# Performance work log

Measured on AMD Instinct MI355X. Metric: run time of the kernel, lower is better.

## Reference

```python
import jax, jax.numpy as jnp
import numpy as np

B = 2048       # batch
D_IN = 512     # input_size
D_MODEL = 1024 # hidden_size / d_model
ED = 2048      # d_inner = 2*d_model
N = 16         # d_state
K = 4          # d_conv
DT = 64        # dt_rank = ceil(d_model/16)
FLAT_H = ED * N
RMS_EPS = 1e-5


def setup_inputs() -> dict:
    key = jax.random.key(0)
    ks = jax.random.split(key, 12)
    rn = lambda k, shape, s: jax.random.normal(k, shape, jnp.float32) * s
    return {
        "x_t": rn(ks[0], (B, D_IN), 1.0),
        "flat_state": rn(ks[1], (B, FLAT_H + ED * (K - 1)), 0.1),
        "W_in_cell": rn(ks[2], (D_MODEL, D_IN), D_IN ** -0.5),
        "norm_w": jnp.ones((D_MODEL,), jnp.float32),
        "W_in": rn(ks[3], (2 * ED, D_MODEL), D_MODEL ** -0.5),
        "conv_w": rn(ks[4], (ED, K), K ** -0.5),  # depthwise conv weight (ED,1,K) squeezed
        "conv_b": rn(ks[5], (ED,), 0.02),
        "W_xproj": rn(ks[6], (DT + 2 * N, ED), ED ** -0.5),
        "W_dt": rn(ks[7], (ED, DT), DT ** -0.5),
        "b_dt": rn(ks[8], (ED,), 0.02),
        "A_log": jnp.log(jnp.broadcast_to(jnp.arange(1, N + 1, dtype=jnp.float32), (ED, N))),
        "D_param": jnp.ones((ED,), jnp.float32),
        "W_out": rn(ks[9], (D_MODEL, ED), ED ** -0.5),
    }


def _rmsnorm(x, w):
    return x * jax.lax.rsqrt(jnp.mean(x * x, axis=-1, keepdims=True) + RMS_EPS) * w


def reference(x_t, flat_state, W_in_cell, norm_w, W_in, conv_w, conv_b,
              W_xproj, W_dt, b_dt, A_log, D_param, W_out):
    # MambaCell.in_proj (bias=False)
    x = x_t @ W_in_cell.T                                  # (B, D_MODEL)
    # unpack flat recurrent state
    h = flat_state[:, :FLAT_H].reshape(B, ED, N)           # SSM state
    inputs = flat_state[:, FLAT_H:].reshape(B, ED, K - 1)  # conv cache

    residual = x
    xn = _rmsnorm(x, norm_w)

    # MambaBlock.step
    xz = xn @ W_in.T                                       # (B, 2*ED)
    x1, z = xz[:, :ED], xz[:, ED:]

    # depthwise causal conv, last output position only
    window = jnp.concatenate([inputs, x1[:, :, None]], axis=2)   # (B, ED, K)
    xc = jnp.einsum("bek,ek->be", window, conv_w) + conv_b
    xs = jax.nn.silu(xc)                                   # (B, ED)

    # selective SSM single step
    dbc = xs @ W_xproj.T                                   # (B, DT+2N)
    delta = jax.nn.softplus(dbc[:, :DT] @ W_dt.T + b_dt)   # (B, ED)
    Bm = dbc[:, DT:DT + N]                                 # (B, N)
    Cm = dbc[:, DT + N:]                                   # (B, N)
    A = -jnp.exp(A_log)                                    # (ED, N)
    dA = jnp.exp(delta[:, :, None] * A[None])              # (B, ED, N)
    dBx = delta[:, :, None] * Bm[:, None, :] * xs[:, :, None]
    h_new = dA * h + dBx                                   # (B, ED, N)
    y = jnp.einsum("ben,bn->be", h_new, Cm) + D_param * xs

    out = (y * jax.nn.silu(z)) @ W_out.T                   # (B, D_MODEL)
    y_t = out + residual                                   # residual connection in ResidualBlock.step

    inputs_new = jnp.concatenate([inputs[:, :, 1:], x1[:, :, None]], axis=2)
    flat_new = jax.lax.stop_gradient(
        jnp.concatenate([h_new.reshape(B, -1), inputs_new.reshape(B, -1)], axis=1))
    return y_t, flat_new
```

## Files before the change

kernel.cpp:

```cpp
#include <hip/hip_runtime.h>
#include <math.h>

#define B 2048
#define D_IN 512
#define D_MODEL 1024
#define ED 2048
#define NSTATE 16
#define KCONV 4
#define DTDIM 64
#define FLAT_H (ED * NSTATE)
#define ROW_STATE (FLAT_H + ED * (KCONV - 1))

typedef __attribute__((ext_vector_type(8))) short short8;
typedef __attribute__((ext_vector_type(4))) short short4v;
typedef __attribute__((ext_vector_type(4))) float f32x4;

__device__ __forceinline__ float sigmoidf_(float x) { return 1.f / (1.f + expf(-x)); }

__device__ __forceinline__ unsigned short f2bf(float f) {
  unsigned u = __float_as_uint(f);
  u += 0x7FFFu + ((u >> 16) & 1u);
  return (unsigned short)(u >> 16);
}
__device__ __forceinline__ float bf2f(unsigned short h) {
  return __uint_as_float((unsigned)h << 16);
}

template <int MODE>
__global__ __launch_bounds__(256) void gemm_nt_mfma(
    const float* __restrict__ A, const float* __restrict__ W,
    float* __restrict__ C, int M, int N, int K, int lda, int ldw, int ldc,
    const float* __restrict__ extra) {
  __shared__ short Ahi[4][128][8];
  __shared__ short Alo[4][128][8];
  __shared__ short Whi[4][128][8];
  __shared__ short Wlo[4][128][8];

  const int tid = threadIdx.x;
  const int lane = tid & 63;
  const int wave = tid >> 6;
  const int wr = wave >> 1;
  const int wc = wave & 1;
  const int m0 = blockIdx.y * 128;
  const int n0 = blockIdx.x * 128;
  const int kg = lane >> 4;
  const int lr = lane & 15;

  f32x4 acc[4][4] = {};

  for (int k0 = 0; k0 < K; k0 += 32) {
#pragma unroll
    for (int it = 0; it < 4; ++it) {
      const int flat = tid + it * 256;
      const int row = flat >> 3;
      const int kq = flat & 7;
      const int tkg = kq >> 1;
      const int j0 = (kq & 1) * 4;
      const float4 av = *(const float4*)(A + (size_t)(m0 + row) * lda + (k0 + kq * 4));
      const float4 wv = *(const float4*)(W + (size_t)(n0 + row) * ldw + (k0 + kq * 4));
      const float af[4] = {av.x, av.y, av.z, av.w};
      const float wf[4] = {wv.x, wv.y, wv.z, wv.w};
      short4v ah, al, wh, wl;
#pragma unroll
      for (int e = 0; e < 4; ++e) {
        const unsigned short h = f2bf(af[e]);
        ah[e] = (short)h;
        al[e] = (short)f2bf(af[e] - bf2f(h));
        const unsigned short hw = f2bf(wf[e]);
        wh[e] = (short)hw;
        wl[e] = (short)f2bf(wf[e] - bf2f(hw));
      }
      *(short4v*)&Ahi[tkg][row][j0] = ah;
      *(short4v*)&Alo[tkg][row][j0] = al;
      *(short4v*)&Whi[tkg][row][j0] = wh;
      *(short4v*)&Wlo[tkg][row][j0] = wl;
    }
    __syncthreads();

    short8 a_h[4], a_l[4], b_h[4], b_l[4];
#pragma unroll
    for (int i = 0; i < 4; ++i) {
      a_h[i] = *(const short8*)&Ahi[kg][wr * 64 + i * 16 + lr][0];
      a_l[i] = *(const short8*)&Alo[kg][wr * 64 + i * 16 + lr][0];
      b_h[i] = *(const short8*)&Whi[kg][wc * 64 + i * 16 + lr][0];
      b_l[i] = *(const short8*)&Wlo[kg][wc * 64 + i * 16 + lr][0];
    }
#pragma unroll
    for (int i = 0; i < 4; ++i)
#pragma unroll
      for (int j = 0; j < 4; ++j) {
        acc[i][j] = __builtin_amdgcn_mfma_f32_16x16x32_bf16(a_h[i], b_h[j], acc[i][j], 0, 0, 0);
        acc[i][j] = __builtin_amdgcn_mfma_f32_16x16x32_bf16(a_l[i], b_h[j], acc[i][j], 0, 0, 0);
        acc[i][j] = __builtin_amdgcn_mfma_f32_16x16x32_bf16(a_h[i], b_l[j], acc[i][j], 0, 0, 0);
      }
    __syncthreads();
  }

#pragma unroll
  for (int i = 0; i < 4; ++i) {
    const int gm = m0 + wr * 64 + i * 16 + kg * 4;
#pragma unroll
    for (int j = 0; j < 4; ++j) {
      const int gn = n0 + wc * 64 + j * 16 + lr;
#pragma unroll
      for (int r = 0; r < 4; ++r) {
        float v = acc[i][j][r];
        if (MODE == 1) {
          v += extra[gn];
          v = (v > 20.f) ? v : log1pf(expf(v));
        } else if (MODE == 2) {
          v += extra[(size_t)(gm + r) * ldc + gn];
        }
        C[(size_t)(gm + r) * ldc + gn] = v;
      }
    }
  }
}

__global__ __launch_bounds__(256) void gemm_nt_splitk(
    const float* __restrict__ A, const float* __restrict__ W,
    float* __restrict__ C, int M, int N, int K, int lda, int ldw, int ldc) {
  __shared__ float As[16][68];
  __shared__ float Ws[16][68];
  const int tid = threadIdx.x;
  const int tx = tid & 15;
  const int ty = tid >> 4;
  const int m0 = blockIdx.y * 64;
  const int n0 = blockIdx.x * 64;
  const int kchunk = K / gridDim.z;
  const int kbeg = blockIdx.z * kchunk;

  float acc[4][4] = {};
  const int lr = tid >> 4;
  const int lc = tid & 15;

  for (int k0 = kbeg; k0 < kbeg + kchunk; k0 += 16) {
#pragma unroll
    for (int i = 0; i < 4; i++) {
      const int r = lr + i * 16;
      const int gk = k0 + lc;
      As[lc][r] = A[(size_t)(m0 + r) * lda + gk];
      const int gn = n0 + r;
      Ws[lc][r] = (gn < N) ? W[(size_t)gn * ldw + gk] : 0.f;
    }
    __syncthreads();
#pragma unroll
    for (int k = 0; k < 16; k++) {
      float a[4], w[4];
#pragma unroll
      for (int i = 0; i < 4; i++) a[i] = As[k][ty * 4 + i];
#pragma unroll
      for (int j = 0; j < 4; j++) w[j] = Ws[k][tx * 4 + j];
#pragma unroll
      for (int i = 0; i < 4; i++)
#pragma unroll
        for (int j = 0; j < 4; j++) acc[i][j] += a[i] * w[j];
    }
    __syncthreads();
  }

#pragma unroll
  for (int i = 0; i < 4; i++) {
    const int gm = m0 + ty * 4 + i;
#pragma unroll
    for (int j = 0; j < 4; j++) {
      const int gn = n0 + tx * 4 + j;
      if (gn >= N) continue;
      atomicAdd(&C[(size_t)gm * ldc + gn], acc[i][j]);
    }
  }
}

__global__ __launch_bounds__(256) void rmsnorm_kernel(
    const float* __restrict__ x, const float* __restrict__ w,
    float* __restrict__ xn) {
  const int b = blockIdx.x;
  const int i4 = threadIdx.x * 4;
  const float4 v = *(const float4*)(x + (size_t)b * D_MODEL + i4);
  float ss = v.x * v.x + v.y * v.y + v.z * v.z + v.w * v.w;
#pragma unroll
  for (int off = 32; off > 0; off >>= 1) ss += __shfl_down(ss, off, 64);
  __shared__ float red[4];
  if ((threadIdx.x & 63) == 0) red[threadIdx.x >> 6] = ss;
  __syncthreads();
  const float tot = red[0] + red[1] + red[2] + red[3];
  const float scale = rsqrtf(tot * (1.f / (float)D_MODEL) + 1e-5f);
  const float4 wv = *(const float4*)(w + i4);
  float4 o;
  o.x = v.x * scale * wv.x;
  o.y = v.y * scale * wv.y;
  o.z = v.z * scale * wv.z;
  o.w = v.w * scale * wv.w;
  *(float4*)(xn + (size_t)b * D_MODEL + i4) = o;
}

__global__ __launch_bounds__(256) void prep_aneg(
    const float* __restrict__ A_log, float* __restrict__ Aneg) {
  const int i4 = (blockIdx.x * 256 + threadIdx.x) * 4;
  const float4 v = *(const float4*)(A_log + i4);
  float4 o;
  o.x = -expf(v.x);
  o.y = -expf(v.y);
  o.z = -expf(v.z);
  o.w = -expf(v.w);
  *(float4*)(Aneg + i4) = o;
}

__global__ __launch_bounds__(256) void conv_silu_kernel(
    const float* __restrict__ flat_state, const float* __restrict__ xz,
    const float* __restrict__ conv_w, const float* __restrict__ conv_b,
    float* __restrict__ xs, float* __restrict__ outFlat) {
  const int b = blockIdx.x;
  __shared__ float sin_[ED * 3];
  __shared__ float sx1[ED];
  const float* inRow = flat_state + (size_t)b * ROW_STATE + FLAT_H;
  const float* x1Row = xz + (size_t)b * (2 * ED);
#pragma unroll
  for (int i = 0; i < 6; ++i) {
    const int idx = (threadIdx.x + i * 256) * 4;
    *(float4*)&sin_[idx] = *(const float4*)&inRow[idx];
  }
#pragma unroll
  for (int i = 0; i < 2; ++i) {
    const int idx = (threadIdx.x + i * 256) * 4;
    *(float4*)&sx1[idx] = *(const float4*)&x1Row[idx];
  }
  __syncthreads();
  float* xsRow = xs + (size_t)b * ED;
#pragma unroll
  for (int k = 0; k < 8; ++k) {
    const int e = threadIdx.x + k * 256;
    const float4 cw = *(const float4*)(conv_w + e * 4);
    const float xc = sin_[e * 3] * cw.x + sin_[e * 3 + 1] * cw.y +
                     sin_[e * 3 + 2] * cw.z + sx1[e] * cw.w + conv_b[e];
    xsRow[e] = xc * sigmoidf_(xc);
  }
  float* on = outFlat + (size_t)b * ROW_STATE + FLAT_H;
#pragma unroll
  for (int k = 0; k < 24; ++k) {
    const int i = threadIdx.x + k * 256;
    const int q = i / 3;
    const int r = i - q * 3;
    on[i] = (r == 2) ? sx1[q] : sin_[i + 1];
  }
}

__global__ __launch_bounds__(256) void state_kernel(
    const float* __restrict__ flat_state, const float* __restrict__ xz,
    const float* __restrict__ xs, const float* __restrict__ dbc,
    const float* __restrict__ delta, const float* __restrict__ Aneg,
    const float* __restrict__ D_param, float* __restrict__ outFlat,
    float* __restrict__ yz) {
  const int id = blockIdx.x * 256 + threadIdx.x;
  const int f = id << 2;
  const int b = f >> 15;
  const int off = f & 32767;
  const int e = off >> 4;
  const int n0 = off & 15;

  const float d = delta[(size_t)b * ED + e];
  const float xsv = xs[(size_t)b * ED + e];
  const float dx = d * xsv;
  const float4 h4 = *(const float4*)(flat_state + (size_t)b * ROW_STATE + off);
  const float4 a4 = *(const float4*)(Aneg + off);
  const float* dbcb = dbc + (size_t)b * 96;
  const float4 B4 = *(const float4*)(dbcb + DTDIM + n0);
  const float4 C4 = *(const float4*)(dbcb + DTDIM + NSTATE + n0);

  float4 hn;
  hn.x = expf(d * a4.x) * h4.x + dx * B4.x;
  hn.y = expf(d * a4.y) * h4.y + dx * B4.y;
  hn.z = expf(d * a4.z) * h4.z + dx * B4.z;
  hn.w = expf(d * a4.w) * h4.w + dx * B4.w;
  *(float4*)(outFlat + (size_t)b * ROW_STATE + off) = hn;

  float y = hn.x * C4.x + hn.y * C4.y + hn.z * C4.z + hn.w * C4.w;
  y += __shfl_xor(y, 1, 64);
  y += __shfl_xor(y, 2, 64);
  if (n0 == 0) {
    y += D_param[e] * xsv;
    const float z = xz[(size_t)b * (2 * ED) + ED + e];
    yz[(size_t)b * ED + e] = y * (z * sigmoidf_(z));
  }
}

extern "C" void kernel_launch(void* const* d_in, const int* in_sizes, int n_in,
                              void* d_out, int out_size, void* d_ws, size_t ws_size,
                              hipStream_t stream) {
  const float* x_t       = (const float*)d_in[0];
  const float* flat_state= (const float*)d_in[1];
  const float* W_in_cell = (const float*)d_in[2];
  const float* norm_w    = (const float*)d_in[3];
  const float* W_in      = (const float*)d_in[4];
  const float* conv_w    = (const float*)d_in[5];
  const float* conv_b    = (const float*)d_in[6];
  const float* W_xproj   = (const float*)d_in[7];
  const float* W_dt      = (const float*)d_in[8];
  const float* b_dt      = (const float*)d_in[9];
  const float* A_log     = (const float*)d_in[10];
  const float* D_param   = (const float*)d_in[11];
  const float* W_out     = (const float*)d_in[12];

  float* y_t_out = (float*)d_out;
  float* outFlat = (float*)d_out + (size_t)B * D_MODEL;

  float* ws = (float*)d_ws;
  float* x     = ws;
  float* xn    = x + (size_t)B * D_MODEL;
  float* xz    = xn + (size_t)B * D_MODEL;
  float* xs    = xz + (size_t)B * 2 * ED;
  float* dbc   = xs + (size_t)B * ED;
  float* delta = dbc + (size_t)B * 96;
  float* yz    = delta + (size_t)B * ED;
  float* Aneg  = xn;

  dim3 blk(256);

  (void)hipMemsetAsync(dbc, 0, (size_t)B * 96 * sizeof(float), stream);

  gemm_nt_mfma<0><<<dim3(D_MODEL / 128, B / 128), blk, 0, stream>>>(
      x_t, W_in_cell, x, B, D_MODEL, D_IN, D_IN, D_IN, D_MODEL, nullptr);
  rmsnorm_kernel<<<dim3(B), blk, 0, stream>>>(x, norm_w, xn);
  gemm_nt_mfma<0><<<dim3(2 * ED / 128, B / 128), blk, 0, stream>>>(
      xn, W_in, xz, B, 2 * ED, D_MODEL, D_MODEL, D_MODEL, 2 * ED, nullptr);
  prep_aneg<<<dim3(ED * NSTATE / 1024), blk, 0, stream>>>(A_log, Aneg);
  conv_silu_kernel<<<dim3(B), blk, 0, stream>>>(
      flat_state, xz, conv_w, conv_b, xs, outFlat);
  gemm_nt_splitk<<<dim3(2, B / 64, 8), blk, 0, stream>>>(
      xs, W_xproj, dbc, B, 96, ED, ED, ED, 96);
  gemm_nt_mfma<1><<<dim3(ED / 128, B / 128), blk, 0, stream>>>(
      dbc, W_dt, delta, B, ED, DTDIM, 96, DTDIM, ED, b_dt);
  state_kernel<<<dim3((size_t)B * FLAT_H / 1024), blk, 0, stream>>>(
      flat_state, xz, xs, dbc, delta, Aneg, D_param, outFlat, yz);
  gemm_nt_mfma<2><<<dim3(D_MODEL / 128, B / 128), blk, 0, stream>>>(
      yz, W_out, y_t_out, B, D_MODEL, ED, ED, ED, D_MODEL, x);
}
```

Baseline: 909.7 us.

## Pre-split operands to bf16 hi/lo and load GEMM tiles via global_load_lds

Adds split kernels that convert the inputs, weights and activations into separate bf16 high and low arrays once. A new GEMM then streams these tiles directly into swizzled LDS with global_load_lds, instead of converting fp32 to split bf16 inside every GEMM tile load. This is meant to remove the repeated per-tile conversion ALU work and halve the global bytes read per operand. In exchange it adds extra launches and extra global traffic for the split passes, including re-splitting the weights on every call.

```diff
diff --git a/kernel.cpp b/kernel.cpp
--- a/kernel.cpp
+++ b/kernel.cpp
@@ -14,6 +14,7 @@
 typedef __attribute__((ext_vector_type(8))) short short8;
 typedef __attribute__((ext_vector_type(4))) short short4v;
 typedef __attribute__((ext_vector_type(4))) float f32x4;
+typedef unsigned short ushort_t;
 
 __device__ __forceinline__ float sigmoidf_(float x) { return 1.f / (1.f + expf(-x)); }
 
@@ -24,6 +25,116 @@
 }
 __device__ __forceinline__ float bf2f(unsigned short h) {
   return __uint_as_float((unsigned)h << 16);
+}
+struct hl_t { short h, l; };
+__device__ __forceinline__ hl_t split2(float f) {
+  hl_t r;
+  const unsigned short hu = f2bf(f);
+  r.h = (short)hu;
+  r.l = (short)f2bf(f - bf2f(hu));
+  return r;
+}
+
+__device__ __forceinline__ void gload_lds16(const void* g, void* l) {
+  __builtin_amdgcn_global_load_lds(
+      (const __attribute__((address_space(1))) void*)g,
+      (__attribute__((address_space(3))) void*)l, 16, 0, 0);
+}
+
+template <int MODE>
+__global__ __launch_bounds__(256) void gemm_bs(
+    const ushort_t* __restrict__ Ahi, const ushort_t* __restrict__ Alo,
+    const ushort_t* __restrict__ Whi, const ushort_t* __restrict__ Wlo,
+    float* __restrict__ C, int M, int N, int K, int ldc,
+    const float* __restrict__ extra) {
+  __shared__ ushort_t lds[2][128][64];
+
+  const int tid = threadIdx.x;
+  const int lane = tid & 63;
+  const int w = tid >> 6;
+  const int wr = w >> 1;
+  const int wc = w & 1;
+  const int m0 = blockIdx.y * 128;
+  const int n0 = blockIdx.x * 128;
+  const int kg = lane >> 4;
+  const int lr = lane & 15;
+
+  const int srow = lane >> 3;
+  const int sslot = lane & 7;
+  const int c = sslot ^ srow;
+  const int mat = c >> 2;
+  const int kq8 = (c & 3) * 8;
+
+  const int side = w >> 1;
+  const ushort_t* hiP = side ? Whi : Ahi;
+  const ushort_t* loP = side ? Wlo : Alo;
+  const ushort_t* matP = mat ? loP : hiP;
+  const int base0 = side ? n0 : m0;
+
+  f32x4 acc[4][4] = {};
+
+  for (int k0 = 0; k0 < K; k0 += 32) {
+#pragma unroll
+    for (int t = 0; t < 8; ++t) {
+      const int rb = (w & 1) * 8 + t;
+      const int row = rb * 8 + srow;
+      const ushort_t* g = matP + (size_t)(base0 + row) * K + k0 + kq8;
+      gload_lds16(g, &lds[side][rb * 8][0]);
+    }
+    __syncthreads();
+
+    short8 a_h[4], a_l[4], b_h[4], b_l[4];
+#pragma unroll
+    for (int i = 0; i < 4; ++i) {
+      const int r = wr * 64 + i * 16 + lr;
+      const int r7 = r & 7;
+      a_h[i] = *(const short8*)&lds[0][r][(kg ^ r7) * 8];
+      a_l[i] = *(const short8*)&lds[0][r][((4 + kg) ^ r7) * 8];
+      const int rr = wc * 64 + i * 16 + lr;
+      const int rr7 = rr & 7;
+      b_h[i] = *(const short8*)&lds[1][rr][(kg ^ rr7) * 8];
+      b_l[i] = *(const short8*)&lds[1][rr][((4 + kg) ^ rr7) * 8];
+    }
+#pragma unroll
+    for (int i = 0; i < 4; ++i)
+#pragma unroll
+      for (int j = 0; j < 4; ++j) {
+        acc[i][j] = __builtin_amdgcn_mfma_f32_16x16x32_bf16(a_h[i], b_h[j], acc[i][j], 0, 0, 0);
+        acc[i][j] = __builtin_amdgcn_mfma_f32_16x16x32_bf16(a_l[i], b_h[j], acc[i][j], 0, 0, 0);
+        acc[i][j] = __builtin_amdgcn_mfma_f32_16x16x32_bf16(a_h[i], b_l[j], acc[i][j], 0, 0, 0);
+      }
+    __syncthreads();
+  }
+
+#pragma unroll
+  for (int i = 0; i < 4; ++i) {
+    const int gm = m0 + wr * 64 + i * 16 + kg * 4;
+#pragma unroll
+    for (int j = 0; j < 4; ++j) {
+      const int gn = n0 + wc * 64 + j * 16 + lr;
+#pragma unroll
+      for (int r = 0; r < 4; ++r) {
+        float v = acc[i][j][r];
+        if (MODE == 2) v += extra[(size_t)(gm + r) * ldc + gn];
+        C[(size_t)(gm + r) * ldc + gn] = v;
+      }
+    }
+  }
+}
+
+__global__ __launch_bounds__(256) void split_kernel(
+    const float* __restrict__ in, ushort_t* __restrict__ hi,
+    ushort_t* __restrict__ lo) {
+  const int i4 = (blockIdx.x * 256 + threadIdx.x) * 4;
+  const float4 v = *(const float4*)(in + i4);
+  short4v h, l;
+  hl_t s0 = split2(v.x), s1 = split2(v.y), s2 = split2(v.z), s3 = split2(v.w);
+  h[0] = s0.h; l[0] = s0.l;
+  h[1] = s1.h; l[1] = s1.l;
+  h[2] = s2.h; l[2] = s2.l;
+  h[3] = s3.h; l[3] = s3.l;
+  *(short4v*)(hi + i4) = h;
+  *(short4v*)(lo + i4) = l;
 }
 
 template <int MODE>
@@ -63,12 +174,10 @@
       short4v ah, al, wh, wl;
 #pragma unroll
       for (int e = 0; e < 4; ++e) {
-        const unsigned short h = f2bf(af[e]);
-        ah[e] = (short)h;
-        al[e] = (short)f2bf(af[e] - bf2f(h));
-        const unsigned short hw = f2bf(wf[e]);
-        wh[e] = (short)hw;
-        wl[e] = (short)f2bf(wf[e] - bf2f(hw));
+        hl_t sa = split2(af[e]);
+        ah[e] = sa.h; al[e] = sa.l;
+        hl_t sw = split2(wf[e]);
+        wh[e] = sw.h; wl[e] = sw.l;
       }
       *(short4v*)&Ahi[tkg][row][j0] = ah;
       *(short4v*)&Alo[tkg][row][j0] = al;
@@ -108,8 +217,6 @@
         if (MODE == 1) {
           v += extra[gn];
           v = (v > 20.f) ? v : log1pf(expf(v));
-        } else if (MODE == 2) {
-          v += extra[(size_t)(gm + r) * ldc + gn];
         }
         C[(size_t)(gm + r) * ldc + gn] = v;
       }
@@ -146,15 +253,15 @@
     __syncthreads();
 #pragma unroll
     for (int k = 0; k < 16; k++) {
-      float a[4], w[4];
+      float a[4], wv[4];
 #pragma unroll
       for (int i = 0; i < 4; i++) a[i] = As[k][ty * 4 + i];
 #pragma unroll
-      for (int j = 0; j < 4; j++) w[j] = Ws[k][tx * 4 + j];
+      for (int j = 0; j < 4; j++) wv[j] = Ws[k][tx * 4 + j];
 #pragma unroll
       for (int i = 0; i < 4; i++)
 #pragma unroll
-        for (int j = 0; j < 4; j++) acc[i][j] += a[i] * w[j];
+        for (int j = 0; j < 4; j++) acc[i][j] += a[i] * wv[j];
     }
     __syncthreads();
   }
@@ -171,9 +278,9 @@
   }
 }
 
-__global__ __launch_bounds__(256) void rmsnorm_kernel(
+__global__ __launch_bounds__(256) void rmsnorm_split_kernel(
     const float* __restrict__ x, const float* __restrict__ w,
-    float* __restrict__ xn) {
+    ushort_t* __restrict__ xn_hi, ushort_t* __restrict__ xn_lo) {
   const int b = blockIdx.x;
   const int i4 = threadIdx.x * 4;
   const float4 v = *(const float4*)(x + (size_t)b * D_MODEL + i4);
@@ -186,12 +293,17 @@
   const float tot = red[0] + red[1] + red[2] + red[3];
   const float scale = rsqrtf(tot * (1.f / (float)D_MODEL) + 1e-5f);
   const float4 wv = *(const float4*)(w + i4);
-  float4 o;
-  o.x = v.x * scale * wv.x;
-  o.y = v.y * scale * wv.y;
-  o.z = v.z * scale * wv.z;
-  o.w = v.w * scale * wv.w;
-  *(float4*)(xn + (size_t)b * D_MODEL + i4) = o;
+  short4v h, l;
+  hl_t s0 = split2(v.x * scale * wv.x);
+  hl_t s1 = split2(v.y * scale * wv.y);
+  hl_t s2 = split2(v.z * scale * wv.z);
+  hl_t s3 = split2(v.w * scale * wv.w);
+  h[0] = s0.h; l[0] = s0.l;
+  h[1] = s1.h; l[1] = s1.l;
+  h[2] = s2.h; l[2] = s2.l;
+  h[3] = s3.h; l[3] = s3.l;
+  *(short4v*)(xn_hi + (size_t)b * D_MODEL + i4) = h;
+  *(short4v*)(xn_lo + (size_t)b * D_MODEL + i4) = l;
 }
 
 __global__ __launch_bounds__(256) void prep_aneg(
@@ -306,24 +418,41 @@
 
   float* ws = (float*)d_ws;
   float* x     = ws;
-  float* xn    = x + (size_t)B * D_MODEL;
-  float* xz    = xn + (size_t)B * D_MODEL;
+  float* xz    = x + (size_t)B * D_MODEL;
   float* xs    = xz + (size_t)B * 2 * ED;
   float* dbc   = xs + (size_t)B * ED;
   float* delta = dbc + (size_t)B * 96;
   float* yz    = delta + (size_t)B * ED;
-  float* Aneg  = xn;
+  float* Aneg  = yz + (size_t)B * ED;
+  ushort_t* us = (ushort_t*)(Aneg + FLAT_H);
+  ushort_t* xt_hi   = us;  us += (size_t)B * D_IN;
+  ushort_t* xt_lo   = us;  us += (size_t)B * D_IN;
+  ushort_t* wic_hi  = us;  us += (size_t)D_MODEL * D_IN;
+  ushort_t* wic_lo  = us;  us += (size_t)D_MODEL * D_IN;
+  ushort_t* win_hi  = us;  us += (size_t)2 * ED * D_MODEL;
+  ushort_t* win_lo  = us;  us += (size_t)2 * ED * D_MODEL;
+  ushort_t* wout_hi = us;  us += (size_t)D_MODEL * ED;
+  ushort_t* wout_lo = us;  us += (size_t)D_MODEL * ED;
+  ushort_t* xn_hi   = us;  us += (size_t)B * D_MODEL;
+  ushort_t* xn_lo   = us;  us += (size_t)B * D_MODEL;
+  ushort_t* yz_hi   = us;  us += (size_t)B * ED;
+  ushort_t* yz_lo   = us;  us += (size_t)B * ED;
 
   dim3 blk(256);
 
   (void)hipMemsetAsync(dbc, 0, (size_t)B * 96 * sizeof(float), stream);
 
-  gemm_nt_mfma<0><<<dim3(D_MODEL / 128, B / 128), blk, 0, stream>>>(
-      x_t, W_in_cell, x, B, D_MODEL, D_IN, D_IN, D_IN, D_MODEL, nullptr);
-  rmsnorm_kernel<<<dim3(B), blk, 0, stream>>>(x, norm_w, xn);
-  gemm_nt_mfma<0><<<dim3(2 * ED / 128, B / 128), blk, 0, stream>>>(
-      xn, W_in, xz, B, 2 * ED, D_MODEL, D_MODEL, D_MODEL, 2 * ED, nullptr);
-  prep_aneg<<<dim3(ED * NSTATE / 1024), blk, 0, stream>>>(A_log, Aneg);
+  split_kernel<<<dim3((B * D_IN) / 1024), blk, 0, stream>>>(x_t, xt_hi, xt_lo);
+  split_kernel<<<dim3((D_MODEL * D_IN) / 1024), blk, 0, stream>>>(W_in_cell, wic_hi, wic_lo);
+  split_kernel<<<dim3((2 * ED * D_MODEL) / 1024), blk, 0, stream>>>(W_in, win_hi, win_lo);
+  split_kernel<<<dim3((D_MODEL * ED) / 1024), blk, 0, stream>>>(W_out, wout_hi, wout_lo);
+
+  gemm_bs<0><<<dim3(D_MODEL / 128, B / 128), blk, 0, stream>>>(
+      xt_hi, xt_lo, wic_hi, wic_lo, x, B, D_MODEL, D_IN, D_MODEL, nullptr);
+  rmsnorm_split_kernel<<<dim3(B), blk, 0, stream>>>(x, norm_w, xn_hi, xn_lo);
+  gemm_bs<0><<<dim3(2 * ED / 128, B / 128), blk, 0, stream>>>(
+      xn_hi, xn_lo, win_hi, win_lo, xz, B, 2 * ED, D_MODEL, 2 * ED, nullptr);
+  prep_aneg<<<dim3(FLAT_H / 1024), blk, 0, stream>>>(A_log, Aneg);
   conv_silu_kernel<<<dim3(B), blk, 0, stream>>>(
       flat_state, xz, conv_w, conv_b, xs, outFlat);
   gemm_nt_splitk<<<dim3(2, B / 64, 8), blk, 0, stream>>>(
@@ -332,6 +461,7 @@
       dbc, W_dt, delta, B, ED, DTDIM, 96, DTDIM, ED, b_dt);
   state_kernel<<<dim3((size_t)B * FLAT_H / 1024), blk, 0, stream>>>(
       flat_state, xz, xs, dbc, delta, Aneg, D_param, outFlat, yz);
-  gemm_nt_mfma<2><<<dim3(D_MODEL / 128, B / 128), blk, 0, stream>>>(
-      yz, W_out, y_t_out, B, D_MODEL, ED, ED, ED, D_MODEL, x);
-}
+  split_kernel<<<dim3((B * ED) / 1024), blk, 0, stream>>>(yz, yz_hi, yz_lo);
+  gemm_bs<2><<<dim3(D_MODEL / 128, B / 128), blk, 0, stream>>>(
+      yz_hi, yz_lo, wout_hi, wout_lo, y_t_out, B, D_MODEL, ED, D_MODEL, x);
+}
```

Measured after the change: 851.9 us. 6.4% less time.
